# Kernel optimization log

Measured on AMD Instinct MI355X. Metric: run time of the kernel, lower is better.

Reference implementation:

```python
import jax, jax.numpy as jnp
import numpy as np


def _tridiag_solve(x, d, l, u):
    # Build dense tridiagonal M (faithful to the torch module) and solve.
    # x: [B, N, F]; d: [F]; l, u: [F-1]
    diag = jax.nn.softplus(d) + 2.0
    M = jnp.diag(diag) + jnp.diag(jnp.tanh(l), -1) + jnp.diag(jnp.tanh(u), 1)
    # solve M @ Y = x^T  -> Y: [B, F, N], then transpose back
    y = jnp.linalg.solve(M, jnp.swapaxes(x, -2, -1))
    return jnp.swapaxes(y, -2, -1)


def setup_inputs() -> dict:
    key = jax.random.key(0)
    ks = jax.random.split(key, 11)
    B, N = 8, 4096
    IN, HID, OUT = 512, 2048, 512
    s = 0.02
    return {
        "x": jax.random.normal(ks[0], (B, N, IN), dtype=jnp.float32),
        "d1": jax.random.normal(ks[1], (IN,), dtype=jnp.float32) * s,
        "l1": jax.random.normal(ks[2], (IN - 1,), dtype=jnp.float32) * s,
        "u1": jax.random.normal(ks[3], (IN - 1,), dtype=jnp.float32) * s,
        "W1": jax.random.normal(ks[4], (HID, IN), dtype=jnp.float32) * s,
        "b1": jax.random.normal(ks[5], (HID,), dtype=jnp.float32) * s,
        "d2": jax.random.normal(ks[6], (HID,), dtype=jnp.float32) * s,
        "l2": jax.random.normal(ks[7], (HID - 1,), dtype=jnp.float32) * s,
        "u2": jax.random.normal(ks[8], (HID - 1,), dtype=jnp.float32) * s,
        "W2": jax.random.normal(ks[9], (OUT, HID), dtype=jnp.float32) * s,
        "b2": jax.random.normal(ks[10], (OUT,), dtype=jnp.float32) * s,
    }


def reference(x, d1, l1, u1, W1, b1, d2, l2, u2, W2, b2):
    h = _tridiag_solve(x, d1, l1, u1)
    h = jax.nn.relu(jnp.einsum("bnf,hf->bnh", h, W1) + b1)
    h = _tridiag_solve(h, d2, l2, u2)
    out = jnp.einsum("bnh,oh->bno", h, W2) + b2
    return out
```

## Files before the change

### kernel.cpp

```cpp
#include <hip/hip_runtime.h>
#include <cstdint>

#define R_ROWS 32768
#define F1 512
#define F2 2048
#define NOUT 512

typedef __bf16 bf16x8 __attribute__((ext_vector_type(8)));
typedef float f32x4 __attribute__((ext_vector_type(4)));

__device__ __forceinline__ float bf2f(uint16_t b) {
  union { uint32_t u; float f; } v; v.u = ((uint32_t)b) << 16; return v.f;
}
__device__ __forceinline__ uint16_t f2bf(float f) {
  union { float f; uint32_t u; } v; v.f = f;
  uint32_t u = v.u;
  return (uint16_t)((u + 0x7fffu + ((u >> 16) & 1u)) >> 16);
}

union U4 { uint4 v; uint16_t s[8]; };

__device__ __forceinline__ int sniff_x(const uint16_t* x) {
  int bad = 0;
  #pragma unroll 8
  for (int i = 0; i < 64; ++i) {
    uint32_t e = (x[i] >> 7) & 0xFFu;
    if (e != 0u && (e < 90u || e > 141u)) bad++;
  }
  return (bad >= 8) ? 1 : 0;
}

__launch_bounds__(256)
__global__ void prep_fused(const void* x,
                           const void* d1, const void* l1, const void* u1,
                           const void* d2, const void* l2, const void* u2,
                           const void* b1, const void* b2,
                           float* f1, float* f2,
                           uint16_t* b1b, uint16_t* b2b, int* flag) {
  const bool inf32 = sniff_x((const uint16_t*)x) != 0;
  if (blockIdx.x == 0 && threadIdx.x == 0) *flag = inf32 ? 1 : 0;
  const int F = blockIdx.x ? F2 : F1;
  float* base = blockIdx.x ? f2 : f1;
  const void* dp = blockIdx.x ? d2 : d1;
  const void* lp = blockIdx.x ? l2 : l1;
  const void* up = blockIdx.x ? u2 : u1;

  __shared__ float sdiag[F2], stl[F2], stu[F2];

  for (int i = threadIdx.x; i < F; i += 256) {
    float dv = inf32 ? ((const float*)dp)[i] : bf2f(((const uint16_t*)dp)[i]);
    sdiag[i] = log1pf(expf(dv)) + 2.0f;
    bool in = i < F - 1;
    float lv = in ? (inf32 ? ((const float*)lp)[i] : bf2f(((const uint16_t*)lp)[i])) : 0.0f;
    float uv = in ? (inf32 ? ((const float*)up)[i] : bf2f(((const uint16_t*)up)[i])) : 0.0f;
    stl[i] = in ? tanhf(lv) : 0.0f;
    stu[i] = in ? tanhf(uv) : 0.0f;
  }
  if (inf32) {
    const float* bsrc = blockIdx.x ? (const float*)b1 : (const float*)b2;
    uint16_t*    bdst = blockIdx.x ? b1b : b2b;
    const int    bn   = blockIdx.x ? F2 : NOUT;
    for (int i = threadIdx.x; i < bn; i += 256) bdst[i] = f2bf(bsrc[i]);
  }
  __syncthreads();

  const int t  = threadIdx.x;
  const int CH = F >> 8;
  const int s0 = t * CH;
  const int j0 = (s0 >= 16) ? (s0 - 16) : 0;
  float b  = sdiag[j0];
  float ib = __builtin_amdgcn_rcpf(b);
  for (int j = j0 + 1; j < s0; ++j) {
    b  = fmaf(-stu[j - 1] * stl[j - 1], ib, sdiag[j]);
    ib = __builtin_amdgcn_rcpf(b);
  }
  #pragma unroll
  for (int q = 0; q < 8; ++q) {
    if (q >= CH) break;
    int i = s0 + q;
    float w, nb;
    if (i == 0) { w = 0.0f; nb = sdiag[0]; }
    else        { w = stu[i - 1] * ib; nb = fmaf(-w, stl[i - 1], sdiag[i]); }
    ib = __builtin_amdgcn_rcpf(nb);
    base[3 * F + i] = w;
    base[4 * F + i] = ib;
    base[5 * F + i] = stl[i] * ib;
  }
}

template<int F>
__device__ void solve_rows(const void* X, uint16_t* Y, const float* fact,
                           bool inf32, int blk,
                           float* sfw, float* sib, float* sbk, uint4* sout) {
  constexpr int LPR = F / 32;
  for (int i = threadIdx.x; i < F; i += 256) {
    int ii = i + (i >> 5);
    sfw[ii] = fact[3 * F + i];
    sib[ii] = fact[4 * F + i];
    sbk[ii] = fact[5 * F + i];
  }
  __syncthreads();
  const int tid = threadIdx.x;
  int gt  = blk * 256 + tid;
  int row = gt / LPR;
  int j   = gt % LPR;
  int k0  = j * 32;
  const size_t rb = (size_t)row * F;

  float xc[32];
  if (inf32) {
    const float* xr = (const float*)X + rb + k0;
    #pragma unroll
    for (int t = 0; t < 8; ++t) {
      float4 v = ((const float4*)xr)[t];
      xc[4*t] = v.x; xc[4*t+1] = v.y; xc[4*t+2] = v.z; xc[4*t+3] = v.w;
    }
  } else {
    const uint16_t* xr = (const uint16_t*)X + rb + k0;
    #pragma unroll
    for (int t = 0; t < 4; ++t) {
      U4 in; in.v = ((const uint4*)xr)[t];
      #pragma unroll
      for (int s = 0; s < 8; ++s) xc[8*t+s] = bf2f(in.s[s]);
    }
  }

  float dp = 0.0f;
  if (j > 0) {
    float xw[16];
    if (inf32) {
      const float* xr = (const float*)X + rb + k0 - 16;
      #pragma unroll
      for (int t = 0; t < 4; ++t) {
        float4 v = ((const float4*)xr)[t];
        xw[4*t] = v.x; xw[4*t+1] = v.y; xw[4*t+2] = v.z; xw[4*t+3] = v.w;
      }
    } else {
      const uint16_t* xr = (const uint16_t*)X + rb + k0 - 16;
      #pragma unroll
      for (int t = 0; t < 2; ++t) {
        U4 in; in.v = ((const uint4*)xr)[t];
        #pragma unroll
        for (int s = 0; s < 8; ++s) xw[8*t+s] = bf2f(in.s[s]);
      }
    }
    #pragma unroll
    for (int t = 0; t < 16; ++t) {
      int k = k0 - 16 + t;
      dp = fmaf(-sfw[k + (k >> 5)], dp, xw[t]);
    }
  }
  float dpv[32];
  #pragma unroll
  for (int t = 0; t < 32; ++t) {
    int k = k0 + t;
    dp = fmaf(-sfw[k + (k >> 5)], dp, xc[t]);
    dpv[t] = dp;
  }

  float wdp[16];
  #pragma unroll
  for (int t = 0; t < 16; ++t) wdp[t] = __shfl_down(dpv[t], 1);
  float yn = 0.0f;
  if (j < LPR - 1) {
    #pragma unroll
    for (int t = 15; t >= 0; --t) {
      int k = k0 + 32 + t;
      int kk = k + (k >> 5);
      yn = fmaf(-sbk[kk], yn, wdp[t] * sib[kk]);
    }
  }
  U4 out[4];
  #pragma unroll
  for (int t = 31; t >= 0; --t) {
    int k = k0 + t;
    int kk = k + (k >> 5);
    yn = fmaf(-sbk[kk], yn, dpv[t] * sib[kk]);
    out[t >> 3].s[t & 7] = f2bf(yn);
  }
  #pragma unroll
  for (int t = 0; t < 4; ++t) sout[tid * 4 + t] = out[t].v;
  __syncthreads();
  uint4* yg = (uint4*)Y + (size_t)blk * 1024;
  #pragma unroll
  for (int i = 0; i < 4; ++i) yg[i * 256 + tid] = sout[i * 256 + tid];
}

#define FP2 (F2 + (F2 >> 5))
__launch_bounds__(256)
__global__ void mid_fused(const void* x, const void* W1, const void* W2,
                          uint16_t* W1s, uint16_t* W2s, uint16_t* xb,
                          const float* f1, const float* f2, const int* flag) {
  __shared__ float sfw[FP2], sib[FP2], sbk[FP2];
  __shared__ uint4 sout[1024];
  const bool inf32 = (*flag == 1);
  const int b = blockIdx.x;
  if (b < 128) {
    solve_rows<F1>(W1, W1s, f1, inf32, b, sfw, sib, sbk, sout);
  } else if (b < 256) {
    solve_rows<F2>(W2, W2s, f2, inf32, b - 128, sfw, sib, sbk, sout);
  } else if (inf32) {
    int q = (b - 256) * 256 + threadIdx.x;
    float4 v = ((const float4*)x)[q];
    ushort4 o;
    o.x = f2bf(v.x); o.y = f2bf(v.y); o.z = f2bf(v.z); o.w = f2bf(v.w);
    ((ushort4*)xb)[q] = o;
  }
}

__device__ __forceinline__ void gl_lds16(const uint16_t* g, uint16_t* l) {
  __builtin_amdgcn_global_load_lds((const __attribute__((address_space(1))) void*)g,
                                   (__attribute__((address_space(3))) void*)l, 16, 0, 0);
}

#define LOFF(bb, ab, h) ((bb) * 32768 + (ab) * 16384 + (h) * 8192)

#define GSTG(gp, bb, ab, h, kt) do {                                              \
    gl_lds16((gp) + (size_t)(h) * 128 * K + (kt),        lds + LOFF(bb, ab, h) + w * 512);        \
    gl_lds16((gp) + ((size_t)(h) * 128 + 64) * K + (kt), lds + LOFF(bb, ab, h) + 4096 + w * 512); \
  } while (0)

#define RD_A(ba, mq) do {                                                         \
    _Pragma("unroll")                                                             \
    for (int fi = 0; fi < 4; ++fi) {                                              \
      af[fi][0] = *(const bf16x8*)(lds + (ba) + (mq) * 8192 + arow + fi * 1024 + c0); \
      af[fi][1] = *(const bf16x8*)(lds + (ba) + (mq) * 8192 + arow + fi * 1024 + c1); \
    }                                                                             \
  } while (0)

#define RD_B(ba, nq) do {                                                         \
    _Pragma("unroll")                                                             \
    for (int fj = 0; fj < 2; ++fj) {                                              \
      bfr[nq][fj][0] = *(const bf16x8*)(lds + (ba) + (nq) * 8192 + brow + fj * 1024 + c0); \
      bfr[nq][fj][1] = *(const bf16x8*)(lds + (ba) + (nq) * 8192 + brow + fj * 1024 + c1); \
    }                                                                             \
  } while (0)

#define MMA_QUAD(mq, nq) do {                                                     \
    _Pragma("unroll")                                                             \
    for (int fi = 0; fi < 4; ++fi) {                                              \
      _Pragma("unroll")                                                           \
      for (int fj = 0; fj < 2; ++fj) {                                            \
        acc[(mq)*4+fi][(nq)*2+fj] = __builtin_amdgcn_mfma_f32_16x16x32_bf16(      \
            af[fi][0], bfr[nq][fj][0], acc[(mq)*4+fi][(nq)*2+fj], 0, 0, 0);       \
        acc[(mq)*4+fi][(nq)*2+fj] = __builtin_amdgcn_mfma_f32_16x16x32_bf16(      \
            af[fi][1], bfr[nq][fj][1], acc[(mq)*4+fi][(nq)*2+fj], 0, 0, 0);       \
      }                                                                           \
    }                                                                             \
  } while (0)

#define VMC(n) asm volatile("s_waitcnt vmcnt(" #n ")" ::: "memory")
#define BAR()  __builtin_amdgcn_s_barrier()
#define SB0()  __builtin_amdgcn_sched_barrier(0)
#define LGKC(n) do { asm volatile("s_waitcnt lgkmcnt(" #n ")" ::: "memory");      \
                     __builtin_amdgcn_sched_barrier(0); } while (0)
#define P1() __builtin_amdgcn_s_setprio(1)
#define P0() __builtin_amdgcn_s_setprio(0)

template<bool RELU, bool FINAL, int NTN>
__launch_bounds__(512, 2)
__global__ void gemm8(const uint16_t* __restrict__ Aa, const uint16_t* __restrict__ Ab,
                      const uint16_t* __restrict__ Bw,
                      const uint16_t* __restrict__ bias0, const uint16_t* __restrict__ bias1,
                      void* __restrict__ Cout, int Nn, int K, const int* flag) {
  __shared__ __align__(16) uint16_t lds[65536];
  const int f = *flag;
  const uint16_t* A    = f ? Ab : Aa;
  const uint16_t* bias = f ? bias1 : bias0;

  const int tid = threadIdx.x;
  const int w = tid >> 6;
  const int l = tid & 63;
  const int wm = w >> 2;
  const int wn = w & 3;

  const int b = blockIdx.x;
  const int x = b & 7;
  const int g = b >> 3;
  const int nb = g & (NTN - 1);
  const int mb = (g / NTN) * 8 + x;
  const int MB = mb * 256, NB = nb * 256;
  const int NT = K >> 6;

  const int srow = w * 8 + (l >> 3);
  const int sch  = (l & 7) ^ ((l >> 3) & 7);
  const uint16_t* ag = A  + (size_t)(MB + srow) * K + sch * 8;
  const uint16_t* bg = Bw + (size_t)(NB + srow) * K + sch * 8;

  const int c0 = (((l >> 4) ^ (l & 7)) << 3);
  const int c1 = c0 ^ 32;
  const int arow = (wm * 64 + (l & 15)) * 64;
  const int brow = (wn * 32 + (l & 15)) * 64;

  f32x4 acc[8][4] = {};
  bf16x8 af[4][2];
  bf16x8 bfr[2][2][2];

  GSTG(ag, 0, 0, 0, 0);
  GSTG(bg, 0, 1, 0, 0);
  GSTG(bg, 0, 1, 1, 0);
  GSTG(ag, 0, 0, 1, 0);
  VMC(2); BAR();

  for (int t = 0; t < NT - 1; ++t) {
    const int cur  = t & 1;
    const int nxt  = cur ^ 1;
    const int curA = cur * 32768;
    const int curB = curA + 16384;
    const int kn   = (t + 1) * 64;

    RD_A(curA, 0); RD_B(curB, 0); RD_B(curB, 1);
    SB0();
    GSTG(ag, nxt, 0, 0, kn);
    GSTG(bg, nxt, 1, 0, kn);
    LGKC(4);  P1(); MMA_QUAD(0, 0); P0();
    LGKC(0);  P1(); MMA_QUAD(0, 1); P0();
    VMC(4); BAR();
    RD_A(curA, 1);
    SB0();
    GSTG(bg, nxt, 1, 1, kn);
    GSTG(ag, nxt, 0, 1, kn);
    LGKC(0);  P1(); MMA_QUAD(1, 0); MMA_QUAD(1, 1); P0();
    VMC(2); BAR();
  }

  {
    const int curA = ((NT - 1) & 1) * 32768;
    const int curB = curA + 16384;
    RD_A(curA, 0); RD_B(curB, 0); RD_B(curB, 1);
    SB0();
    LGKC(4);  P1(); MMA_QUAD(0, 0); P0();
    LGKC(0);  P1(); MMA_QUAD(0, 1); P0();
    VMC(0); BAR();
    RD_A(curA, 1);
    LGKC(0);  P1(); MMA_QUAD(1, 0); MMA_QUAD(1, 1); P0();
  }

  const bool outf32 = FINAL && (f != 0);
  const int ccol  = l & 15;
  const int crow4 = (l >> 4) * 4;
  #pragma unroll
  for (int j = 0; j < 4; ++j) {
    int gcol = NB + (j >> 1) * 128 + wn * 32 + (j & 1) * 16 + ccol;
    float bv = bf2f(bias[gcol]);
    #pragma unroll
    for (int i = 0; i < 8; ++i) {
      int grow = MB + (i >> 2) * 128 + wm * 64 + (i & 3) * 16 + crow4;
      #pragma unroll
      for (int rr = 0; rr < 4; ++rr) {
        float v = acc[i][j][rr] + bv;
        if (RELU) v = fmaxf(v, 0.0f);
        size_t idx = (size_t)(grow + rr) * Nn + gcol;
        if (outf32) ((float*)Cout)[idx]    = v;
        else        ((uint16_t*)Cout)[idx] = f2bf(v);
      }
    }
  }
}

extern "C" void kernel_launch(void* const* d_in, const int* in_sizes, int n_in,
                              void* d_out, int out_size, void* d_ws, size_t ws_size,
                              hipStream_t stream) {
  const void* x  = d_in[0];
  const void* d1 = d_in[1];
  const void* l1 = d_in[2];
  const void* u1 = d_in[3];
  const void* W1 = d_in[4];
  const void* b1 = d_in[5];
  const void* d2 = d_in[6];
  const void* l2 = d_in[7];
  const void* u2 = d_in[8];
  const void* W2 = d_in[9];
  const void* b2 = d_in[10];

  char* ws = (char*)d_ws;
  int*      flag = (int*)ws;
  float*    f1   = (float*)(ws + 256);
  float*    f2   = (float*)(ws + (64 << 10));
  uint16_t* b1b  = (uint16_t*)(ws + (128 << 10));
  uint16_t* b2b  = (uint16_t*)(ws + (136 << 10));
  uint16_t* W1s  = (uint16_t*)(ws + (1 << 20));
  uint16_t* W2s  = (uint16_t*)(ws + (3 << 20));
  uint16_t* xb   = (uint16_t*)(ws + ((size_t)8 << 20));
  uint16_t* H1   = (uint16_t*)(ws + ((size_t)40 << 20));

  prep_fused<<<2, 256, 0, stream>>>(x, d1, l1, u1, d2, l2, u2, b1, b2,
                                    f1, f2, b1b, b2b, flag);

  mid_fused<<<256 + (R_ROWS * F1 / 4) / 256, 256, 0, stream>>>(
      x, W1, W2, W1s, W2s, xb, f1, f2, flag);

  gemm8<true, false, 8><<<1024, 512, 0, stream>>>(
      (const uint16_t*)x, xb, W1s, (const uint16_t*)b1, b1b, H1, F2, F1, flag);

  gemm8<false, true, 2><<<256, 512, 0, stream>>>(
      H1, H1, W2s, (const uint16_t*)b2, b2b, d_out, NOUT, F2, flag);
}
```

Baseline: 309.1 us.

## Restructure GEMM main loop to prefetch next-tile LDS fragments and grid-stride conversion

The GEMM k-loop now issues all four global-to-LDS stages for the next tile up front. It reads the remaining fragments of the current tile, then after a single barrier preloads the first A/B fragments of the next tile into registers, so LDS reads overlap the previous iteration's tail. A-fragments are double-buffered in registers (afr[2][4][2]), and the waitcnt points are reorganized to a single full drain per iteration. Separately, the x fp32-to-bf16 conversion in mid_fused becomes a grid-stride loop over 1024 blocks instead of launching one block per 1024 elements. The extra fragment registers may pressure occupancy at 2 waves/SIMD, and using one barrier with full vmcnt drain may reduce global load overlap.

```diff
diff --git a/kernel.cpp b/kernel.cpp
--- a/kernel.cpp
+++ b/kernel.cpp
@@ -200,11 +200,13 @@
   } else if (b < 256) {
     solve_rows<F2>(W2, W2s, f2, inf32, b - 128, sfw, sib, sbk, sout);
   } else if (inf32) {
-    int q = (b - 256) * 256 + threadIdx.x;
-    float4 v = ((const float4*)x)[q];
-    ushort4 o;
-    o.x = f2bf(v.x); o.y = f2bf(v.y); o.z = f2bf(v.z); o.w = f2bf(v.w);
-    ((ushort4*)xb)[q] = o;
+    const int NQ = R_ROWS * F1 / 4;
+    for (int q = (b - 256) * 256 + threadIdx.x; q < NQ; q += 1024 * 256) {
+      float4 v = ((const float4*)x)[q];
+      ushort4 o;
+      o.x = f2bf(v.x); o.y = f2bf(v.y); o.z = f2bf(v.z); o.w = f2bf(v.w);
+      ((ushort4*)xb)[q] = o;
+    }
   }
 }
 
@@ -223,8 +225,8 @@
 #define RD_A(ba, mq) do {                                                         \
     _Pragma("unroll")                                                             \
     for (int fi = 0; fi < 4; ++fi) {                                              \
-      af[fi][0] = *(const bf16x8*)(lds + (ba) + (mq) * 8192 + arow + fi * 1024 + c0); \
-      af[fi][1] = *(const bf16x8*)(lds + (ba) + (mq) * 8192 + arow + fi * 1024 + c1); \
+      afr[mq][fi][0] = *(const bf16x8*)(lds + (ba) + (mq) * 8192 + arow + fi * 1024 + c0); \
+      afr[mq][fi][1] = *(const bf16x8*)(lds + (ba) + (mq) * 8192 + arow + fi * 1024 + c1); \
     }                                                                             \
   } while (0)
 
@@ -242,9 +244,9 @@
       _Pragma("unroll")                                                           \
       for (int fj = 0; fj < 2; ++fj) {                                            \
         acc[(mq)*4+fi][(nq)*2+fj] = __builtin_amdgcn_mfma_f32_16x16x32_bf16(      \
-            af[fi][0], bfr[nq][fj][0], acc[(mq)*4+fi][(nq)*2+fj], 0, 0, 0);       \
+            afr[mq][fi][0], bfr[nq][fj][0], acc[(mq)*4+fi][(nq)*2+fj], 0, 0, 0);  \
         acc[(mq)*4+fi][(nq)*2+fj] = __builtin_amdgcn_mfma_f32_16x16x32_bf16(      \
-            af[fi][1], bfr[nq][fj][1], acc[(mq)*4+fi][(nq)*2+fj], 0, 0, 0);       \
+            afr[mq][fi][1], bfr[nq][fj][1], acc[(mq)*4+fi][(nq)*2+fj], 0, 0, 0);  \
       }                                                                           \
     }                                                                             \
   } while (0)
@@ -293,46 +295,54 @@
   const int brow = (wn * 32 + (l & 15)) * 64;
 
   f32x4 acc[8][4] = {};
-  bf16x8 af[4][2];
+  bf16x8 afr[2][4][2];
   bf16x8 bfr[2][2][2];
 
   GSTG(ag, 0, 0, 0, 0);
   GSTG(bg, 0, 1, 0, 0);
   GSTG(bg, 0, 1, 1, 0);
   GSTG(ag, 0, 0, 1, 0);
-  VMC(2); BAR();
+  VMC(0); BAR();
+  LGKC(0);
+  RD_A(0, 0); RD_B(16384, 0);
+  SB0();
 
   for (int t = 0; t < NT - 1; ++t) {
     const int cur  = t & 1;
     const int nxt  = cur ^ 1;
     const int curA = cur * 32768;
     const int curB = curA + 16384;
+    const int nxtA = nxt * 32768;
+    const int nxtB = nxtA + 16384;
     const int kn   = (t + 1) * 64;
 
-    RD_A(curA, 0); RD_B(curB, 0); RD_B(curB, 1);
-    SB0();
     GSTG(ag, nxt, 0, 0, kn);
     GSTG(bg, nxt, 1, 0, kn);
-    LGKC(4);  P1(); MMA_QUAD(0, 0); P0();
-    LGKC(0);  P1(); MMA_QUAD(0, 1); P0();
-    VMC(4); BAR();
-    RD_A(curA, 1);
-    SB0();
     GSTG(bg, nxt, 1, 1, kn);
     GSTG(ag, nxt, 0, 1, kn);
+    SB0();
+    RD_B(curB, 1);
+    SB0();
+    RD_A(curA, 1);
+    SB0();
+    LGKC(12); P1(); MMA_QUAD(0, 0); P0();
+    LGKC(8);  P1(); MMA_QUAD(0, 1); P0();
     LGKC(0);  P1(); MMA_QUAD(1, 0); MMA_QUAD(1, 1); P0();
-    VMC(2); BAR();
+    VMC(0); BAR();
+    SB0();
+    RD_A(nxtA, 0); RD_B(nxtB, 0);
+    SB0();
   }
 
   {
     const int curA = ((NT - 1) & 1) * 32768;
     const int curB = curA + 16384;
-    RD_A(curA, 0); RD_B(curB, 0); RD_B(curB, 1);
-    SB0();
-    LGKC(4);  P1(); MMA_QUAD(0, 0); P0();
-    LGKC(0);  P1(); MMA_QUAD(0, 1); P0();
-    VMC(0); BAR();
+    RD_B(curB, 1);
+    SB0();
     RD_A(curA, 1);
+    SB0();
+    LGKC(12); P1(); MMA_QUAD(0, 0); P0();
+    LGKC(8);  P1(); MMA_QUAD(0, 1); P0();
     LGKC(0);  P1(); MMA_QUAD(1, 0); MMA_QUAD(1, 1); P0();
   }
 
@@ -387,7 +397,7 @@
   prep_fused<<<2, 256, 0, stream>>>(x, d1, l1, u1, d2, l2, u2, b1, b2,
                                     f1, f2, b1b, b2b, flag);
 
-  mid_fused<<<256 + (R_ROWS * F1 / 4) / 256, 256, 0, stream>>>(
+  mid_fused<<<1280, 256, 0, stream>>>(
       x, W1, W2, W1s, W2s, xb, f1, f2, flag);
 
   gemm8<true, false, 8><<<1024, 512, 0, stream>>>(
```

New measurement: 309.0 us. About the same (-0.0%).
